# Optimization experiments

Hardware: AMD Instinct MI355X
Metric: run time of the kernel (lower is better)

Reference implementation:

```python
import jax, jax.numpy as jnp
import numpy as np

B, N, K = 16, 100000, 8


def compute_laplacian(x, nbs_idxs, nbs_weights):
    # x: [B, N, 3]; nbs_idxs: [N, K]; nbs_weights: [N, K]
    gathered = x[:, nbs_idxs]  # [B, N, K, 3]
    return x + (gathered * nbs_weights[None, :, :, None]).sum(axis=2)


def setup_inputs() -> dict:
    key = jax.random.key(0)
    k1, k2, k3, k4 = jax.random.split(key, 4)
    geom = jax.random.normal(k1, (B, N, 3), dtype=jnp.float32)
    geom_template_posed = jax.random.normal(k2, (B, N, 3), dtype=jnp.float32)
    nbs_idxs = jax.random.randint(k3, (N, K), 0, N, dtype=jnp.int32)
    nbs_weights = jax.random.normal(k4, (N, K), dtype=jnp.float32)
    return {
        "geom": geom,
        "geom_template_posed": geom_template_posed,
        "nbs_idxs": nbs_idxs,
        "nbs_weights": nbs_weights,
    }


def reference(geom, geom_template_posed, nbs_idxs, nbs_weights):
    l_preds = compute_laplacian(geom, nbs_idxs, nbs_weights)
    # targets side is detached in the original (stop_gradient)
    l_targets = compute_laplacian(jax.lax.stop_gradient(geom_template_posed), nbs_idxs, nbs_weights)
    diff = l_preds - l_targets
    return jnp.mean(diff * diff)
```

## Files before the change

kernel.cpp:

```cpp
#include <hip/hip_runtime.h>

#define BB 16
#define NN 100000
#define KK 8
#define BLOCK 256

#define ROW_U4 8
#define DT_BYTES ((size_t)NN * 128)
#define GRID1 ((NN + 63) / 64)
#define TPV 8
#define GRID2 (NN * TPV / BLOCK)
#define SCALE (1.0f / ((float)BB * NN * 3))

__device__ __forceinline__ unsigned pk_bf16(float a, float b) {
    unsigned ua = __float_as_uint(a), ub = __float_as_uint(b);
    ua = (ua + 0x7FFFu + ((ua >> 16) & 1u)) >> 16;
    ub = (ub + 0x7FFFu + ((ub >> 16) & 1u)) >> 16;
    return ua | (ub << 16);
}

__device__ __forceinline__ void fma8(float* a, uint4 u, float wv) {
    a[0] += wv * __uint_as_float(u.x << 16);
    a[1] += wv * __uint_as_float(u.x & 0xFFFF0000u);
    a[2] += wv * __uint_as_float(u.y << 16);
    a[3] += wv * __uint_as_float(u.y & 0xFFFF0000u);
    a[4] += wv * __uint_as_float(u.z << 16);
    a[5] += wv * __uint_as_float(u.z & 0xFFFF0000u);
    a[6] += wv * __uint_as_float(u.w << 16);
    a[7] += wv * __uint_as_float(u.w & 0xFFFF0000u);
}

__global__ __launch_bounds__(BLOCK) void diff_transpose_bf16_kernel(
    const float4* __restrict__ geom4,
    const float4* __restrict__ gtp4,
    uint4*        __restrict__ dT4)
{
    __shared__ float tile[64][49];
    int tid = threadIdx.x;
    int b = tid >> 4;
    int q = tid & 15;
    int nbase = blockIdx.x * 64;
    int n0 = nbase + q * 4;

    if (n0 < NN) {
        int fi = (b * (NN * 3) + n0 * 3) >> 2;
        float4 g0 = geom4[fi], g1 = geom4[fi + 1], g2 = geom4[fi + 2];
        float4 t0 = gtp4[fi],  t1 = gtp4[fi + 1],  t2 = gtp4[fi + 2];
        float d[12] = {g0.x - t0.x, g0.y - t0.y, g0.z - t0.z, g0.w - t0.w,
                       g1.x - t1.x, g1.y - t1.y, g1.z - t1.z, g1.w - t1.w,
                       g2.x - t2.x, g2.y - t2.y, g2.z - t2.z, g2.w - t2.w};
        #pragma unroll
        for (int e = 0; e < 12; ++e)
            tile[q * 4 + e / 3][b * 3 + e % 3] = d[e];
    }
    __syncthreads();

    #pragma unroll
    for (int i = 0; i < 2; ++i) {
        int t2 = i * BLOCK + tid;
        int r = t2 >> 3, m = t2 & 7;
        int n = nbase + r;
        if (n < NN) {
            uint4 o;
            if (m < 6) {
                const float* row = &tile[r][m * 8];
                o.x = pk_bf16(row[0], row[1]);
                o.y = pk_bf16(row[2], row[3]);
                o.z = pk_bf16(row[4], row[5]);
                o.w = pk_bf16(row[6], row[7]);
            } else {
                o.x = o.y = o.z = o.w = 0u;
            }
            dT4[n * ROW_U4 + m] = o;
        }
    }
}

__global__ __launch_bounds__(BLOCK) void lap_gather_kernel(
    const uint4* __restrict__ dv,
    const int*   __restrict__ idx,
    const float* __restrict__ w,
    float*       __restrict__ partial)
{
    int t = blockIdx.x * BLOCK + threadIdx.x;
    int n = t >> 3;
    int s = t & 7;

    float a[8];
    #pragma unroll
    for (int i = 0; i < 8; ++i) a[i] = 0.0f;

    fma8(a, dv[n * ROW_U4 + s], 1.0f);

    const int4*   ip = reinterpret_cast<const int4*>(idx + (size_t)n * KK);
    const float4* wp = reinterpret_cast<const float4*>(w + (size_t)n * KK);
    int4   i0 = ip[0], i1 = ip[1];
    float4 w0 = wp[0], w1 = wp[1];
    int   js[KK] = {i0.x, i0.y, i0.z, i0.w, i1.x, i1.y, i1.z, i1.w};
    float wk[KK] = {w0.x, w0.y, w0.z, w0.w, w1.x, w1.y, w1.z, w1.w};

    #pragma unroll
    for (int k = 0; k < KK; ++k)
        fma8(a, dv[js[k] * ROW_U4 + s], wk[k]);

    float ssq = 0.0f;
    #pragma unroll
    for (int i = 0; i < 8; ++i) ssq += a[i] * a[i];

    #pragma unroll
    for (int off = 32; off > 0; off >>= 1)
        ssq += __shfl_down(ssq, off, 64);

    __shared__ float wsum[BLOCK / 64];
    int lane = threadIdx.x & 63;
    int wid  = threadIdx.x >> 6;
    if (lane == 0) wsum[wid] = ssq;
    __syncthreads();

    if (threadIdx.x == 0)
        partial[blockIdx.x] = wsum[0] + wsum[1] + wsum[2] + wsum[3];
}

__global__ __launch_bounds__(BLOCK) void final_reduce_kernel(
    const float* __restrict__ partial,
    float*       __restrict__ out)
{
    float s = 0.0f;
    for (int i = threadIdx.x; i < GRID2; i += BLOCK)
        s += partial[i];

    #pragma unroll
    for (int off = 32; off > 0; off >>= 1)
        s += __shfl_down(s, off, 64);

    __shared__ float wsum[BLOCK / 64];
    int lane = threadIdx.x & 63;
    int wid  = threadIdx.x >> 6;
    if (lane == 0) wsum[wid] = s;
    __syncthreads();

    if (threadIdx.x == 0)
        out[0] = (wsum[0] + wsum[1] + wsum[2] + wsum[3]) * SCALE;
}

extern "C" void kernel_launch(void* const* d_in, const int* in_sizes, int n_in,
                              void* d_out, int out_size, void* d_ws, size_t ws_size,
                              hipStream_t stream) {
    const float* geom = (const float*)d_in[0];
    const float* gtp  = (const float*)d_in[1];
    const int*   idx  = (const int*)d_in[2];
    const float* w    = (const float*)d_in[3];
    float* out = (float*)d_out;

    uint4* dT4     = (uint4*)d_ws;
    float* partial = (float*)((char*)d_ws + DT_BYTES);

    diff_transpose_bf16_kernel<<<GRID1, BLOCK, 0, stream>>>(
        (const float4*)geom, (const float4*)gtp, dT4);
    lap_gather_kernel<<<GRID2, BLOCK, 0, stream>>>(dT4, idx, w, partial);
    final_reduce_kernel<<<1, BLOCK, 0, stream>>>(partial, out);
}
```

Baseline: 32.43 us.

## Store transposed diff as fp8 and fuse final reduction via atomics

Packs the per-vertex diff row as fp8 instead of bf16, halving the row to 64 bytes so each gathered neighbour costs half the memory traffic, with four threads per vertex instead of eight. It also drops the separate final-reduce kernel: each block atomically adds its scaled partial sum into the output, which the first kernel zeroes. The fp8 quantisation adds a lot of numerical error on the random inputs and may break tolerance. The atomic accumulation makes the float sum order nondeterministic.

```diff
diff --git a/kernel.cpp b/kernel.cpp
--- a/kernel.cpp
+++ b/kernel.cpp
@@ -5,35 +5,38 @@
 #define KK 8
 #define BLOCK 256
 
-#define ROW_U4 8
-#define DT_BYTES ((size_t)NN * 128)
+#define ROW_U4 4
+#define DT_BYTES ((size_t)NN * 64)
 #define GRID1 ((NN + 63) / 64)
-#define TPV 8
-#define GRID2 (NN * TPV / BLOCK)
+#define TPV 4
+#define GRID2 ((NN * TPV + BLOCK - 1) / BLOCK)
 #define SCALE (1.0f / ((float)BB * NN * 3))
 
-__device__ __forceinline__ unsigned pk_bf16(float a, float b) {
-    unsigned ua = __float_as_uint(a), ub = __float_as_uint(b);
-    ua = (ua + 0x7FFFu + ((ua >> 16) & 1u)) >> 16;
-    ub = (ub + 0x7FFFu + ((ub >> 16) & 1u)) >> 16;
-    return ua | (ub << 16);
+typedef float f32x2 __attribute__((ext_vector_type(2)));
+
+__device__ __forceinline__ unsigned pk_fp8x4(float a, float b, float c, float d) {
+    int v = __builtin_amdgcn_cvt_pk_fp8_f32(a, b, 0, false);
+    v     = __builtin_amdgcn_cvt_pk_fp8_f32(c, d, v, true);
+    return (unsigned)v;
 }
 
-__device__ __forceinline__ void fma8(float* a, uint4 u, float wv) {
-    a[0] += wv * __uint_as_float(u.x << 16);
-    a[1] += wv * __uint_as_float(u.x & 0xFFFF0000u);
-    a[2] += wv * __uint_as_float(u.y << 16);
-    a[3] += wv * __uint_as_float(u.y & 0xFFFF0000u);
-    a[4] += wv * __uint_as_float(u.z << 16);
-    a[5] += wv * __uint_as_float(u.z & 0xFFFF0000u);
-    a[6] += wv * __uint_as_float(u.w << 16);
-    a[7] += wv * __uint_as_float(u.w & 0xFFFF0000u);
+__device__ __forceinline__ void fma16(float* a, uint4 u, float wv) {
+    f32x2 p;
+    p = __builtin_amdgcn_cvt_pk_f32_fp8((int)u.x, false); a[0]  += wv * p.x; a[1]  += wv * p.y;
+    p = __builtin_amdgcn_cvt_pk_f32_fp8((int)u.x, true ); a[2]  += wv * p.x; a[3]  += wv * p.y;
+    p = __builtin_amdgcn_cvt_pk_f32_fp8((int)u.y, false); a[4]  += wv * p.x; a[5]  += wv * p.y;
+    p = __builtin_amdgcn_cvt_pk_f32_fp8((int)u.y, true ); a[6]  += wv * p.x; a[7]  += wv * p.y;
+    p = __builtin_amdgcn_cvt_pk_f32_fp8((int)u.z, false); a[8]  += wv * p.x; a[9]  += wv * p.y;
+    p = __builtin_amdgcn_cvt_pk_f32_fp8((int)u.z, true ); a[10] += wv * p.x; a[11] += wv * p.y;
+    p = __builtin_amdgcn_cvt_pk_f32_fp8((int)u.w, false); a[12] += wv * p.x; a[13] += wv * p.y;
+    p = __builtin_amdgcn_cvt_pk_f32_fp8((int)u.w, true ); a[14] += wv * p.x; a[15] += wv * p.y;
 }
 
-__global__ __launch_bounds__(BLOCK) void diff_transpose_bf16_kernel(
+__global__ __launch_bounds__(BLOCK) void diff_transpose_fp8_kernel(
     const float4* __restrict__ geom4,
     const float4* __restrict__ gtp4,
-    uint4*        __restrict__ dT4)
+    uint4*        __restrict__ dT4,
+    float*        __restrict__ out)
 {
     __shared__ float tile[64][49];
     int tid = threadIdx.x;
@@ -41,6 +44,8 @@
     int q = tid & 15;
     int nbase = blockIdx.x * 64;
     int n0 = nbase + q * 4;
+
+    if (blockIdx.x == 0 && tid == 0) out[0] = 0.0f;
 
     if (n0 < NN) {
         int fi = (b * (NN * 3) + n0 * 3) >> 2;
@@ -55,19 +60,17 @@
     }
     __syncthreads();
 
-    #pragma unroll
-    for (int i = 0; i < 2; ++i) {
-        int t2 = i * BLOCK + tid;
-        int r = t2 >> 3, m = t2 & 7;
+    {
+        int r = tid >> 2, m = tid & 3;
         int n = nbase + r;
         if (n < NN) {
             uint4 o;
-            if (m < 6) {
-                const float* row = &tile[r][m * 8];
-                o.x = pk_bf16(row[0], row[1]);
-                o.y = pk_bf16(row[2], row[3]);
-                o.z = pk_bf16(row[4], row[5]);
-                o.w = pk_bf16(row[6], row[7]);
+            if (m < 3) {
+                const float* row = &tile[r][m * 16];
+                o.x = pk_fp8x4(row[0],  row[1],  row[2],  row[3]);
+                o.y = pk_fp8x4(row[4],  row[5],  row[6],  row[7]);
+                o.z = pk_fp8x4(row[8],  row[9],  row[10], row[11]);
+                o.w = pk_fp8x4(row[12], row[13], row[14], row[15]);
             } else {
                 o.x = o.y = o.z = o.w = 0u;
             }
@@ -80,32 +83,34 @@
     const uint4* __restrict__ dv,
     const int*   __restrict__ idx,
     const float* __restrict__ w,
-    float*       __restrict__ partial)
+    float*       __restrict__ out)
 {
     int t = blockIdx.x * BLOCK + threadIdx.x;
-    int n = t >> 3;
-    int s = t & 7;
-
-    float a[8];
-    #pragma unroll
-    for (int i = 0; i < 8; ++i) a[i] = 0.0f;
-
-    fma8(a, dv[n * ROW_U4 + s], 1.0f);
-
-    const int4*   ip = reinterpret_cast<const int4*>(idx + (size_t)n * KK);
-    const float4* wp = reinterpret_cast<const float4*>(w + (size_t)n * KK);
-    int4   i0 = ip[0], i1 = ip[1];
-    float4 w0 = wp[0], w1 = wp[1];
-    int   js[KK] = {i0.x, i0.y, i0.z, i0.w, i1.x, i1.y, i1.z, i1.w};
-    float wk[KK] = {w0.x, w0.y, w0.z, w0.w, w1.x, w1.y, w1.z, w1.w};
-
-    #pragma unroll
-    for (int k = 0; k < KK; ++k)
-        fma8(a, dv[js[k] * ROW_U4 + s], wk[k]);
+    int n = t >> 2;
+    int s = t & 3;
 
     float ssq = 0.0f;
-    #pragma unroll
-    for (int i = 0; i < 8; ++i) ssq += a[i] * a[i];
+    if (n < NN) {
+        float a[16];
+        #pragma unroll
+        for (int i = 0; i < 16; ++i) a[i] = 0.0f;
+
+        fma16(a, dv[n * ROW_U4 + s], 1.0f);
+
+        const int4*   ip = reinterpret_cast<const int4*>(idx + (size_t)n * KK);
+        const float4* wp = reinterpret_cast<const float4*>(w + (size_t)n * KK);
+        int4   i0 = ip[0], i1 = ip[1];
+        float4 w0 = wp[0], w1 = wp[1];
+        int   js[KK] = {i0.x, i0.y, i0.z, i0.w, i1.x, i1.y, i1.z, i1.w};
+        float wk[KK] = {w0.x, w0.y, w0.z, w0.w, w1.x, w1.y, w1.z, w1.w};
+
+        #pragma unroll
+        for (int k = 0; k < KK; ++k)
+            fma16(a, dv[js[k] * ROW_U4 + s], wk[k]);
+
+        #pragma unroll
+        for (int i = 0; i < 16; ++i) ssq += a[i] * a[i];
+    }
 
     #pragma unroll
     for (int off = 32; off > 0; off >>= 1)
@@ -117,30 +122,9 @@
     if (lane == 0) wsum[wid] = ssq;
     __syncthreads();
 
-    if (threadIdx.x == 0)
-        partial[blockIdx.x] = wsum[0] + wsum[1] + wsum[2] + wsum[3];
-}
-
-__global__ __launch_bounds__(BLOCK) void final_reduce_kernel(
-    const float* __restrict__ partial,
-    float*       __restrict__ out)
-{
-    float s = 0.0f;
-    for (int i = threadIdx.x; i < GRID2; i += BLOCK)
-        s += partial[i];
-
-    #pragma unroll
-    for (int off = 32; off > 0; off >>= 1)
-        s += __shfl_down(s, off, 64);
-
-    __shared__ float wsum[BLOCK / 64];
-    int lane = threadIdx.x & 63;
-    int wid  = threadIdx.x >> 6;
-    if (lane == 0) wsum[wid] = s;
-    __syncthreads();
-
-    if (threadIdx.x == 0)
-        out[0] = (wsum[0] + wsum[1] + wsum[2] + wsum[3]) * SCALE;
+    if (threadIdx.x == 0) {
+        atomicAdd(out, (wsum[0] + wsum[1] + wsum[2] + wsum[3]) * SCALE);
+    }
 }
 
 extern "C" void kernel_launch(void* const* d_in, const int* in_sizes, int n_in,
@@ -152,11 +136,9 @@
     const float* w    = (const float*)d_in[3];
     float* out = (float*)d_out;
 
-    uint4* dT4     = (uint4*)d_ws;
-    float* partial = (float*)((char*)d_ws + DT_BYTES);
+    uint4* dT4 = (uint4*)d_ws;
 
-    diff_transpose_bf16_kernel<<<GRID1, BLOCK, 0, stream>>>(
-        (const float4*)geom, (const float4*)gtp, dT4);
-    lap_gather_kernel<<<GRID2, BLOCK, 0, stream>>>(dT4, idx, w, partial);
-    final_reduce_kernel<<<1, BLOCK, 0, stream>>>(partial, out);
+    diff_transpose_fp8_kernel<<<GRID1, BLOCK, 0, stream>>>(
+        (const float4*)geom, (const float4*)gtp, dT4, out);
+    lap_gather_kernel<<<GRID2, BLOCK, 0, stream>>>(dT4, idx, w, out);
 }
```

Result: slower. 38.25 us (+17.9%).
